# Performance work log

Hardware: AMD Instinct MI355X
Metric: run time of the kernel (lower is better)

Reference implementation:

```python
import jax, jax.numpy as jnp
import numpy as np

N_CODES = 65536  # 2**(n_bits*codebook_dim) = 2**(2*8)
CB_DIM = 8


def setup_inputs() -> dict:
    key = jax.random.key(0)
    k1, k2 = jax.random.split(key)
    x = jax.random.normal(k1, (16, 2048), dtype=jnp.float32)
    codebook = jax.random.normal(k2, (N_CODES, CB_DIM), dtype=jnp.float32)
    return {"x": x, "codebook": codebook}


def reference(x, codebook):
    # per-row scaling factor (detached in torch; forward value identical)
    scale = jnp.mean(jnp.abs(x), axis=1, keepdims=True)  # [B, 1]
    u = x / scale
    flat = u.reshape(-1, codebook.shape[1])  # [M, d]

    # squared euclidean distances (argmin is identical to cdist argmin)
    d2 = (
        jnp.sum(flat * flat, axis=1, keepdims=True)
        - 2.0 * flat @ codebook.T
        + jnp.sum(codebook * codebook, axis=1)
    )  # [M, N]
    indices = jnp.argmin(d2, axis=1)  # [M]

    # EMA-style codebook replacement: cluster means with count clamp
    sums = jax.ops.segment_sum(flat, indices, num_segments=codebook.shape[0])
    counts = jax.ops.segment_sum(
        jnp.ones((flat.shape[0],), dtype=jnp.float32), indices,
        num_segments=codebook.shape[0])
    new_codebook = sums / jnp.clip(counts, 1.0, None)[:, None]

    quantized = new_codebook[indices].reshape(x.shape)
    return scale * quantized
```

## Files before the change

### kernel.cpp

```cpp
#include <hip/hip_runtime.h>
#include <stdint.h>

#define N_CODES 65536
#define CB_DIM 8
#define B_ROWS 16
#define X_COLS 2048
#define M_ROWS 4096
#define RPB 8
#define THREADS 256

#define WS_SCALE 0
#define WS_IDX   256
#define WS_NU    16640
#define WS_SUMS  147712
#define WS_CNT   2244864

#define CODE_BODY(C0, C1, NIDX)                                            \
    {                                                                      \
        float hn = (C0).x * (C0).x;                                        \
        hn = fmaf((C0).y, (C0).y, hn);                                     \
        hn = fmaf((C0).z, (C0).z, hn);                                     \
        hn = fmaf((C0).w, (C0).w, hn);                                     \
        hn = fmaf((C1).x, (C1).x, hn);                                     \
        hn = fmaf((C1).y, (C1).y, hn);                                     \
        hn = fmaf((C1).z, (C1).z, hn);                                     \
        hn = fmaf((C1).w, (C1).w, hn);                                     \
        _Pragma("unroll")                                                  \
        for (int r = 0; r < RPB; r++) {                                    \
            float d = hn;                                                  \
            d = fmaf(nu[r * 8 + 0], (C0).x, d);                            \
            d = fmaf(nu[r * 8 + 1], (C0).y, d);                            \
            d = fmaf(nu[r * 8 + 2], (C0).z, d);                            \
            d = fmaf(nu[r * 8 + 3], (C0).w, d);                            \
            d = fmaf(nu[r * 8 + 4], (C1).x, d);                            \
            d = fmaf(nu[r * 8 + 5], (C1).y, d);                            \
            d = fmaf(nu[r * 8 + 6], (C1).z, d);                            \
            d = fmaf(nu[r * 8 + 7], (C1).w, d);                            \
            if (d < best[r]) { best[r] = d; bidx[r] = (NIDX); }            \
        }                                                                  \
    }

__global__ __launch_bounds__(256) void prep_kernel(const float* __restrict__ x,
                                                   float* __restrict__ scale_out,
                                                   float* __restrict__ nu_out) {
    int row = blockIdx.x;
    int tid = threadIdx.x;
    const float4* xv = (const float4*)(x + row * X_COLS);
    float4 q0 = xv[tid];
    float4 q1 = xv[tid + 256];
    float s = fabsf(q0.x) + fabsf(q0.y) + fabsf(q0.z) + fabsf(q0.w)
            + fabsf(q1.x) + fabsf(q1.y) + fabsf(q1.z) + fabsf(q1.w);
    #pragma unroll
    for (int off = 32; off > 0; off >>= 1) s += __shfl_down(s, off, 64);
    __shared__ float ls[4];
    __shared__ float scale_sh;
    int wave = tid >> 6, lane = tid & 63;
    if (lane == 0) ls[wave] = s;
    __syncthreads();
    if (tid == 0) {
        float t = (ls[0] + ls[1] + ls[2] + ls[3]) * (1.0f / (float)X_COLS);
        scale_sh = t;
        scale_out[row] = t;
    }
    __syncthreads();
    float sc = scale_sh;

    float4 n0, n1;
    n0.x = -2.0f * (q0.x / sc); n0.y = -2.0f * (q0.y / sc);
    n0.z = -2.0f * (q0.z / sc); n0.w = -2.0f * (q0.w / sc);
    n1.x = -2.0f * (q1.x / sc); n1.y = -2.0f * (q1.y / sc);
    n1.z = -2.0f * (q1.z / sc); n1.w = -2.0f * (q1.w / sc);
    float4* nv = (float4*)(nu_out + row * X_COLS);
    nv[tid] = n0;
    nv[tid + 256] = n1;
}

__global__ __launch_bounds__(256, 2) void argmin_kernel(const float* __restrict__ cb,
                                                        const float* __restrict__ nu_g,
                                                        int* __restrict__ indices,
                                                        float* __restrict__ sums,
                                                        float* __restrict__ counts) {
    int tid = threadIdx.x;
    int m0 = blockIdx.x * RPB;

    const float* nup = nu_g + (size_t)m0 * CB_DIM;
    float nu[RPB * CB_DIM];
    #pragma unroll
    for (int i = 0; i < RPB * CB_DIM; i++) nu[i] = nup[i];

    float best[RPB];
    int   bidx[RPB];
    #pragma unroll
    for (int r = 0; r < RPB; r++) { best[r] = 3.4e38f; bidx[r] = 0; }

    const float4* cp = (const float4*)cb;
    float4 a0 = cp[2 * tid],             a1 = cp[2 * tid + 1];
    float4 b0 = cp[2 * (tid + THREADS)], b1 = cp[2 * (tid + THREADS) + 1];

    int n = tid;
    for (int k = 0; k < 127; k++, n += 2 * THREADS) {
        float4 pa0 = cp[2 * (n + 2 * THREADS)], pa1 = cp[2 * (n + 2 * THREADS) + 1];
        CODE_BODY(a0, a1, n)
        float4 pb0 = cp[2 * (n + 3 * THREADS)], pb1 = cp[2 * (n + 3 * THREADS) + 1];
        CODE_BODY(b0, b1, n + THREADS)
        a0 = pa0; a1 = pa1; b0 = pb0; b1 = pb1;
    }
    CODE_BODY(a0, a1, n)
    CODE_BODY(b0, b1, n + THREADS)

    __shared__ unsigned long long red[RPB][THREADS];
    #pragma unroll
    for (int r = 0; r < RPB; r++) {
        unsigned int b = __float_as_uint(best[r]);
        unsigned int k = b ^ ((unsigned int)((int)b >> 31) | 0x80000000u);
        red[r][tid] = ((unsigned long long)k << 32) | (unsigned int)bidx[r];
    }
    for (int t = THREADS / 2; t > 0; t >>= 1) {
        __syncthreads();
        if (tid < t) {
            #pragma unroll
            for (int r = 0; r < RPB; r++) {
                unsigned long long a = red[r][tid], c = red[r][tid + t];
                if (c < a) red[r][tid] = c;
            }
        }
    }
    __syncthreads();

    if (tid < RPB) {
        int idx = (int)(red[tid][0] & 0xFFFFFFFFull);
        indices[m0 + tid] = idx;
        counts[idx] = 0.f;
        float4 z = make_float4(0.f, 0.f, 0.f, 0.f);
        float4* sp = (float4*)(sums + (size_t)idx * CB_DIM);
        sp[0] = z;
        sp[1] = z;
    }
}

__global__ __launch_bounds__(256) void accum_kernel(const int* __restrict__ indices,
                                                    const float* __restrict__ nu_g,
                                                    float* __restrict__ sums,
                                                    float* __restrict__ counts) {
    int m = blockIdx.x * blockDim.x + threadIdx.x;
    if (m < M_ROWS) {
        int idx = indices[m];
        atomicAdd(&counts[idx], 1.0f);
        #pragma unroll
        for (int k = 0; k < CB_DIM; k++)
            atomicAdd(&sums[(size_t)idx * CB_DIM + k], -0.5f * nu_g[m * CB_DIM + k]);
    }
}

__global__ __launch_bounds__(256) void gather_kernel(const int* __restrict__ indices,
                                                     const float* __restrict__ sums,
                                                     const float* __restrict__ counts,
                                                     const float* __restrict__ scale,
                                                     float* __restrict__ out) {
    int e = blockIdx.x * blockDim.x + threadIdx.x;
    if (e < B_ROWS * X_COLS) {
        int m = e >> 3, k = e & 7;
        int idx = indices[m];
        float c = counts[idx];
        c = c < 1.f ? 1.f : c;
        out[e] = scale[e >> 11] * (sums[(size_t)idx * CB_DIM + k] / c);
    }
}

extern "C" void kernel_launch(void* const* d_in, const int* in_sizes, int n_in,
                              void* d_out, int out_size, void* d_ws, size_t ws_size,
                              hipStream_t stream) {
    const float* x  = (const float*)d_in[0];
    const float* cb = (const float*)d_in[1];
    char* ws = (char*)d_ws;
    float* scale   = (float*)(ws + WS_SCALE);
    int*   indices = (int*)(ws + WS_IDX);
    float* nu      = (float*)(ws + WS_NU);
    float* sums    = (float*)(ws + WS_SUMS);
    float* counts  = (float*)(ws + WS_CNT);
    float* out     = (float*)d_out;

    prep_kernel  <<<B_ROWS, 256, 0, stream>>>(x, scale, nu);
    argmin_kernel<<<M_ROWS / RPB, 256, 0, stream>>>(cb, nu, indices, sums, counts);
    accum_kernel <<<M_ROWS / 256, 256, 0, stream>>>(indices, nu, sums, counts);
    gather_kernel<<<(B_ROWS * X_COLS) / 256, 256, 0, stream>>>(indices, sums, counts, scale, out);
}
```

Before: 165.8 us.

## Replace atomic scatter and gather with per-row match-scan finalize kernel

Drops the atomic segment-sum accumulation and the separate gather kernel. A single finalize kernel loads all indices into shared memory, and for each row scans every index to sum the vectors sharing its code, then writes the scaled mean directly. This removes one launch and the contended global atomics, at the cost of redundant O(M^2) compare work per block. The argmin kernel also drops from 8 to 4 rows per block with a higher occupancy bound, doubling the number of blocks.

```diff
diff --git a/kernel.cpp b/kernel.cpp
--- a/kernel.cpp
+++ b/kernel.cpp
@@ -6,14 +6,12 @@
 #define B_ROWS 16
 #define X_COLS 2048
 #define M_ROWS 4096
-#define RPB 8
+#define RPB 4
 #define THREADS 256
 
 #define WS_SCALE 0
 #define WS_IDX   256
 #define WS_NU    16640
-#define WS_SUMS  147712
-#define WS_CNT   2244864
 
 #define CODE_BODY(C0, C1, NIDX)                                            \
     {                                                                      \
@@ -75,11 +73,9 @@
     nv[tid + 256] = n1;
 }
 
-__global__ __launch_bounds__(256, 2) void argmin_kernel(const float* __restrict__ cb,
+__global__ __launch_bounds__(256, 4) void argmin_kernel(const float* __restrict__ cb,
                                                         const float* __restrict__ nu_g,
-                                                        int* __restrict__ indices,
-                                                        float* __restrict__ sums,
-                                                        float* __restrict__ counts) {
+                                                        int* __restrict__ indices) {
     int tid = threadIdx.x;
     int m0 = blockIdx.x * RPB;
 
@@ -126,44 +122,83 @@
         }
     }
     __syncthreads();
-
     if (tid < RPB) {
-        int idx = (int)(red[tid][0] & 0xFFFFFFFFull);
-        indices[m0 + tid] = idx;
-        counts[idx] = 0.f;
-        float4 z = make_float4(0.f, 0.f, 0.f, 0.f);
-        float4* sp = (float4*)(sums + (size_t)idx * CB_DIM);
-        sp[0] = z;
-        sp[1] = z;
-    }
-}
-
-__global__ __launch_bounds__(256) void accum_kernel(const int* __restrict__ indices,
-                                                    const float* __restrict__ nu_g,
-                                                    float* __restrict__ sums,
-                                                    float* __restrict__ counts) {
-    int m = blockIdx.x * blockDim.x + threadIdx.x;
-    if (m < M_ROWS) {
-        int idx = indices[m];
-        atomicAdd(&counts[idx], 1.0f);
+        indices[m0 + tid] = (int)(red[tid][0] & 0xFFFFFFFFull);
+    }
+}
+
+__global__ __launch_bounds__(256) void finalize_kernel(const int* __restrict__ indices,
+                                                       const float* __restrict__ nu_g,
+                                                       const float* __restrict__ scale,
+                                                       float* __restrict__ out) {
+    __shared__ int idx_sh[M_ROWS];
+    int tid = threadIdx.x;
+    {
+        const int4* ig = (const int4*)indices;
+        int4* is = (int4*)idx_sh;
+        for (int i = tid; i < M_ROWS / 4; i += 256) is[i] = ig[i];
+    }
+    __syncthreads();
+
+    int r = tid >> 3, p = tid & 7;
+    int m = blockIdx.x * 32 + r;
+    int my = idx_sh[m];
+
+    float cnt = 0.f;
+    float sum[CB_DIM];
+    #pragma unroll
+    for (int k = 0; k < CB_DIM; k++) sum[k] = 0.f;
+
+    const float4* uv = (const float4*)nu_g;
+    const int4* is = (const int4*)(idx_sh + p * 512);
+    #pragma unroll 2
+    for (int q = 0; q < 128; q++) {
+        int4 w = is[q];
+        int j = p * 512 + 4 * q;
+        if (w.x == my) {
+            float4 v0 = uv[2 * j], v1 = uv[2 * j + 1];
+            cnt += 1.f;
+            sum[0] += v0.x; sum[1] += v0.y; sum[2] += v0.z; sum[3] += v0.w;
+            sum[4] += v1.x; sum[5] += v1.y; sum[6] += v1.z; sum[7] += v1.w;
+        }
+        if (w.y == my) {
+            float4 v0 = uv[2 * j + 2], v1 = uv[2 * j + 3];
+            cnt += 1.f;
+            sum[0] += v0.x; sum[1] += v0.y; sum[2] += v0.z; sum[3] += v0.w;
+            sum[4] += v1.x; sum[5] += v1.y; sum[6] += v1.z; sum[7] += v1.w;
+        }
+        if (w.z == my) {
+            float4 v0 = uv[2 * j + 4], v1 = uv[2 * j + 5];
+            cnt += 1.f;
+            sum[0] += v0.x; sum[1] += v0.y; sum[2] += v0.z; sum[3] += v0.w;
+            sum[4] += v1.x; sum[5] += v1.y; sum[6] += v1.z; sum[7] += v1.w;
+        }
+        if (w.w == my) {
+            float4 v0 = uv[2 * j + 6], v1 = uv[2 * j + 7];
+            cnt += 1.f;
+            sum[0] += v0.x; sum[1] += v0.y; sum[2] += v0.z; sum[3] += v0.w;
+            sum[4] += v1.x; sum[5] += v1.y; sum[6] += v1.z; sum[7] += v1.w;
+        }
+    }
+
+    #pragma unroll
+    for (int off = 1; off < 8; off <<= 1) {
+        cnt += __shfl_xor(cnt, off, 64);
         #pragma unroll
-        for (int k = 0; k < CB_DIM; k++)
-            atomicAdd(&sums[(size_t)idx * CB_DIM + k], -0.5f * nu_g[m * CB_DIM + k]);
-    }
-}
-
-__global__ __launch_bounds__(256) void gather_kernel(const int* __restrict__ indices,
-                                                     const float* __restrict__ sums,
-                                                     const float* __restrict__ counts,
-                                                     const float* __restrict__ scale,
-                                                     float* __restrict__ out) {
-    int e = blockIdx.x * blockDim.x + threadIdx.x;
-    if (e < B_ROWS * X_COLS) {
-        int m = e >> 3, k = e & 7;
-        int idx = indices[m];
-        float c = counts[idx];
-        c = c < 1.f ? 1.f : c;
-        out[e] = scale[e >> 11] * (sums[(size_t)idx * CB_DIM + k] / c);
+        for (int k = 0; k < CB_DIM; k++) sum[k] += __shfl_xor(sum[k], off, 64);
+    }
+
+    if (p == 0) {
+        float c = cnt < 1.f ? 1.f : cnt;
+        float sc = scale[m >> 8];
+        float inv = -0.5f / c;
+        float4 o0 = make_float4(sc * (sum[0] * inv), sc * (sum[1] * inv),
+                                sc * (sum[2] * inv), sc * (sum[3] * inv));
+        float4 o1 = make_float4(sc * (sum[4] * inv), sc * (sum[5] * inv),
+                                sc * (sum[6] * inv), sc * (sum[7] * inv));
+        float4* op = (float4*)(out + (size_t)m * CB_DIM);
+        op[0] = o0;
+        op[1] = o1;
     }
 }
 
@@ -176,12 +211,9 @@
     float* scale   = (float*)(ws + WS_SCALE);
     int*   indices = (int*)(ws + WS_IDX);
     float* nu      = (float*)(ws + WS_NU);
-    float* sums    = (float*)(ws + WS_SUMS);
-    float* counts  = (float*)(ws + WS_CNT);
     float* out     = (float*)d_out;
 
-    prep_kernel  <<<B_ROWS, 256, 0, stream>>>(x, scale, nu);
-    argmin_kernel<<<M_ROWS / RPB, 256, 0, stream>>>(cb, nu, indices, sums, counts);
-    accum_kernel <<<M_ROWS / 256, 256, 0, stream>>>(indices, nu, sums, counts);
-    gather_kernel<<<(B_ROWS * X_COLS) / 256, 256, 0, stream>>>(indices, sums, counts, scale, out);
-}
+    prep_kernel    <<<B_ROWS, 256, 0, stream>>>(x, scale, nu);
+    argmin_kernel  <<<M_ROWS / RPB, 256, 0, stream>>>(cb, nu, indices);
+    finalize_kernel<<<M_ROWS / 32, 256, 0, stream>>>(indices, nu, scale, out);
+}
```

Measured after the change: 171.4 us. +3.4%, slower.
